# Optimization experiments

Hardware: AMD Instinct MI355X
Metric: run time of the kernel (lower is better)

## Reference

```python
import jax, jax.numpy as jnp
import numpy as np

DIM = 3
SIGMA_MIN = 0.05
NORM_EPS = 1e-10
DEG2RAD = np.pi / 180.0


def setup_inputs() -> dict:
    key = jax.random.key(0)
    kF, = jax.random.split(key, 1)
    B = 4_000_000
    F = jax.random.normal(kF, (B, 3, 3), dtype=jnp.float32)
    return {
        "F": F,
        "youngs_modulus_log": jnp.asarray(np.log(2_000_000.0), dtype=jnp.float32),
        "poissons_ratio": jnp.asarray(0.4, dtype=jnp.float32),
        "friction_angle": jnp.asarray(25.0, dtype=jnp.float32),
        "cohesion": jnp.asarray(0.0, dtype=jnp.float32),
    }


def reference(F, youngs_modulus_log, poissons_ratio, friction_angle, cohesion):
    E = jnp.exp(youngs_modulus_log)
    sin_phi = jnp.sin(friction_angle * DEG2RAD)
    alpha = jnp.sqrt(2.0 / 3.0) * 2.0 * sin_phi / (3.0 - sin_phi)
    mu = E / (2.0 * (1.0 + poissons_ratio))
    la = E * poissons_ratio / ((1.0 + poissons_ratio) * (1.0 - 2.0 * poissons_ratio))

    # Batched 3x3 SVD: U (B,3,3), sigma (B,3), Vh (B,3,3)
    U, sigma, Vh = jnp.linalg.svd(F, full_matrices=False)

    sigma = jnp.maximum(sigma, SIGMA_MIN)
    eps = jnp.log(sigma)                                   # log strain (B,3)
    trace = eps.sum(axis=1, keepdims=True)                 # (B,1)
    eps_hat = eps - trace / DIM                            # deviatoric part
    eps_hat_norm = jnp.maximum(
        jnp.linalg.norm(eps_hat, axis=1, keepdims=True), NORM_EPS)
    shifted_trace = trace - cohesion * DIM
    cond_yield = shifted_trace < 0.0                       # (B,1)
    delta_gamma = eps_hat_norm + (DIM * la + 2.0 * mu) / (2.0 * mu) * shifted_trace * alpha
    compress_eps = eps - jnp.maximum(delta_gamma, 0.0) / eps_hat_norm * eps_hat
    expand_eps = jnp.ones_like(eps) * cohesion
    eps_corrected = jnp.where(cond_yield, compress_eps, expand_eps)

    # F_corrected = U @ diag(exp(eps_corrected)) @ Vh
    F_corrected = jnp.einsum('bij,bj,bjk->bik', U, jnp.exp(eps_corrected), Vh)
    return F_corrected
```

## Files before the change

### kernel.cpp

```cpp
#include <hip/hip_runtime.h>
#include <math.h>

#define BLOCK 256
#define F4PB (BLOCK * 9 / 4)

__device__ __forceinline__ float frcp(float x)  { return __builtin_amdgcn_rcpf(x); }
__device__ __forceinline__ float frsq(float x)  { return __builtin_amdgcn_rsqf(x); }
__device__ __forceinline__ float fsqrt_r(float x){ return __builtin_amdgcn_sqrtf(x); }

__device__ __forceinline__ void rot(
    float& x0, float& x1, float& x2, float& np,
    float& y0, float& y1, float& y2, float& nq)
{
    float apq = fmaf(x0, y0, fmaf(x1, y1, x2 * y2));
    float del = np - nq;
    float rho = apq + apq;
    float r   = fsqrt_r(fmaf(del, del, rho * rho));
    float ch  = fabsf(del) + r + 1e-15f;
    bool  sw  = del < 0.0f;
    float sh  = sw ? -rho : rho;
    float inv = frsq(fmaf(ch, ch, sh * sh));
    float c   = ch * inv;
    float s   = sh * inv;
    float cf  = sw ? -s : c;
    float sf  = sw ?  c : s;
    float t;
    t = x0; x0 = fmaf(cf, t, sf * y0); y0 = fmaf(cf, y0, -sf * t);
    t = x1; x1 = fmaf(cf, t, sf * y1); y1 = fmaf(cf, y1, -sf * t);
    t = x2; x2 = fmaf(cf, t, sf * y2); y2 = fmaf(cf, y2, -sf * t);
    float sum = np + nq;
    np = 0.5f * (sum + r);
    nq = fmaxf(0.5f * (sum - r), 0.0f);
}

__global__ __launch_bounds__(BLOCK) void dp_kernel(
    const float* __restrict__ F,
    const float* __restrict__ p_yml,
    const float* __restrict__ p_nu,
    const float* __restrict__ p_fa,
    const float* __restrict__ p_coh,
    float* __restrict__ out,
    int n_elem)
{
    __shared__ float lds[BLOCK * 9];
    const int t_id    = threadIdx.x;
    const int nfloats = n_elem * 9;
    const int base_f  = (int)blockIdx.x * (BLOCK * 9);

    #pragma unroll
    for (int j = 0; j < 3; ++j) {
        int idx = t_id + j * BLOCK;
        if (idx < F4PB) {
            int g4 = (base_f >> 2) + idx;
            int gf = g4 << 2;
            if (gf + 4 <= nfloats) {
                ((float4*)lds)[idx] = ((const float4*)F)[g4];
            } else {
                #pragma unroll
                for (int k = 0; k < 4; ++k)
                    if (gf + k < nfloats) lds[idx * 4 + k] = F[gf + k];
            }
        }
    }
    __syncthreads();

    const int  e     = (int)blockIdx.x * BLOCK + t_id;
    const bool valid = e < n_elem;

    float a00, a01, a02, a10, a11, a12, a20, a21, a22;
    {
        const float* p = lds + t_id * 9;
        a00 = p[0]; a01 = p[1]; a02 = p[2];
        a10 = p[3]; a11 = p[4]; a12 = p[5];
        a20 = p[6]; a21 = p[7]; a22 = p[8];
    }

    const float yml = p_yml[0];
    const float nu  = p_nu[0];
    const float fa  = p_fa[0];
    const float coh = p_coh[0];
    const float E     = __expf(yml);
    const float sphi  = __sinf(fa * 0.017453292519943295f);
    const float alpha = 1.632993161855452f * sphi * frcp(3.0f - sphi);
    const float mu    = E * 0.5f * frcp(1.0f + nu);
    const float la    = E * nu * frcp((1.0f + nu) * (1.0f - 2.0f * nu));
    const float ratio = (3.0f * la + 2.0f * mu) * frcp(2.0f * mu) * alpha;

    float c00=a00, c10=a10, c20=a20;
    float c01=a01, c11=a11, c21=a21;
    float c02=a02, c12=a12, c22=a22;
    float n0 = fmaf(c00,c00, fmaf(c10,c10, c20*c20));
    float n1 = fmaf(c01,c01, fmaf(c11,c11, c21*c21));
    float n2 = fmaf(c02,c02, fmaf(c12,c12, c22*c22));

    #pragma unroll
    for (int sweep = 0; sweep < 4; ++sweep) {
        rot(c00,c10,c20,n0, c01,c11,c21,n1);
        rot(c00,c10,c20,n0, c02,c12,c22,n2);
        rot(c01,c11,c21,n1, c02,c12,c22,n2);
    }

    float i0 = frsq(fmaxf(n0, 1e-30f));
    float i1 = frsq(fmaxf(n1, 1e-30f));
    float u00 = c00*i0, u10 = c10*i0, u20 = c20*i0;
    float u01 = c01*i1, u11 = c11*i1, u21 = c21*i1;
    float u02 = fmaf(u10,u21, -u20*u11);
    float u12 = fmaf(u20,u01, -u00*u21);
    float u22 = fmaf(u00,u11, -u10*u01);

    float q0 = fmaf(a00,u00, fmaf(a10,u10, a20*u20));
    float q1 = fmaf(a01,u00, fmaf(a11,u10, a21*u20));
    float q2 = fmaf(a02,u00, fmaf(a12,u10, a22*u20));
    float m0 = fmaf(q0,q0, fmaf(q1,q1, q2*q2));
    float j0 = frsq(fmaxf(m0, 1e-30f));
    float v00 = q0*j0, v10 = q1*j0, v20 = q2*j0;

    q0 = fmaf(a00,u01, fmaf(a10,u11, a20*u21));
    q1 = fmaf(a01,u01, fmaf(a11,u11, a21*u21));
    q2 = fmaf(a02,u01, fmaf(a12,u11, a22*u21));
    float m1 = fmaf(q0,q0, fmaf(q1,q1, q2*q2));
    float j1 = frsq(fmaxf(m1, 1e-30f));
    float v01 = q0*j1, v11 = q1*j1, v21 = q2*j1;

    float v02 = fmaf(v10,v21, -v20*v11);
    float v12 = fmaf(v20,v01, -v00*v21);
    float v22 = fmaf(v00,v11, -v10*v01);

    float w0 = fmaf(a00,v02, fmaf(a01,v12, a02*v22));
    float w1 = fmaf(a10,v02, fmaf(a11,v12, a12*v22));
    float w2 = fmaf(a20,v02, fmaf(a21,v12, a22*v22));
    float s2 = fmaf(u02,w0, fmaf(u12,w1, u22*w2));

    float e0 = 0.5f * __logf(fmaxf(n0, 0.0025f));
    float e1 = 0.5f * __logf(fmaxf(n1, 0.0025f));
    float e2 = __logf(fmaxf(fabsf(s2), 0.05f));
    float tr  = e0 + e1 + e2;
    float tr3 = tr * (1.0f / 3.0f);
    float h0 = e0 - tr3, h1 = e1 - tr3, h2 = e2 - tr3;
    float hn = fsqrt_r(fmaf(h0,h0, fmaf(h1,h1, h2*h2)));
    hn = fmaxf(hn, 1e-10f);
    float st = tr - coh * 3.0f;
    float dg = hn + ratio * st;
    float sc = fmaxf(dg, 0.0f) * frcp(hn);
    bool yield = st < 0.0f;
    float ec0 = yield ? fmaf(-sc, h0, e0) : coh;
    float ec1 = yield ? fmaf(-sc, h1, e1) : coh;
    float ec2 = yield ? fmaf(-sc, h2, e2) : coh;
    float f0 = __expf(ec0);
    float f1 = __expf(ec1);
    float f2 = copysignf(__expf(ec2), s2);

    float w00 = u00*f0, w01 = u01*f1, w02 = u02*f2;
    float w10 = u10*f0, w11 = u11*f1, w12 = u12*f2;
    float w20 = u20*f0, w21 = u21*f1, w22 = u22*f2;
    float r00 = fmaf(w00,v00, fmaf(w01,v01, w02*v02));
    float r01 = fmaf(w00,v10, fmaf(w01,v11, w02*v12));
    float r02 = fmaf(w00,v20, fmaf(w01,v21, w02*v22));
    float r10 = fmaf(w10,v00, fmaf(w11,v01, w12*v02));
    float r11 = fmaf(w10,v10, fmaf(w11,v11, w12*v12));
    float r12 = fmaf(w10,v20, fmaf(w11,v21, w12*v22));
    float r20 = fmaf(w20,v00, fmaf(w21,v01, w22*v02));
    float r21 = fmaf(w20,v10, fmaf(w21,v11, w22*v12));
    float r22 = fmaf(w20,v20, fmaf(w21,v21, w22*v22));

    __syncthreads();
    if (valid) {
        float* p = lds + t_id * 9;
        p[0]=r00; p[1]=r01; p[2]=r02;
        p[3]=r10; p[4]=r11; p[5]=r12;
        p[6]=r20; p[7]=r21; p[8]=r22;
    }
    __syncthreads();

    #pragma unroll
    for (int j = 0; j < 3; ++j) {
        int idx = t_id + j * BLOCK;
        if (idx < F4PB) {
            int g4 = (base_f >> 2) + idx;
            int gf = g4 << 2;
            if (gf + 4 <= nfloats) {
                ((float4*)out)[g4] = ((float4*)lds)[idx];
            } else {
                #pragma unroll
                for (int k = 0; k < 4; ++k)
                    if (gf + k < nfloats) out[gf + k] = lds[idx * 4 + k];
            }
        }
    }
}

extern "C" void kernel_launch(void* const* d_in, const int* in_sizes, int n_in,
                              void* d_out, int out_size, void* d_ws, size_t ws_size,
                              hipStream_t stream) {
    const float* F = (const float*)d_in[0];
    const int n_elem = in_sizes[0] / 9;
    const int grid = (n_elem + BLOCK - 1) / BLOCK;
    dp_kernel<<<grid, BLOCK, 0, stream>>>(
        F,
        (const float*)d_in[1], (const float*)d_in[2],
        (const float*)d_in[3], (const float*)d_in[4],
        (float*)d_out, n_elem);
}
```

Baseline: 255.9 us.

## Replace Jacobi SVD with closed-form eigen solve, two elements per thread

Swaps the 4-sweep one-sided Jacobi SVD for an analytic eigendecomposition of F^T F (trigonometric cubic roots with a polynomial acos, plus cross-product eigenvectors), then recovers U from A·V. Each thread now handles two elements through a paired-float struct that the compiler may map to packed FP32 math. The LDS-staged coalesced float4 load/store is replaced by direct strided 9-float global accesses per element. The closed form can lose accuracy for nearly repeated or tiny singular values, and the uncoalesced memory access may hurt bandwidth on this memory-bound-sized problem.

```diff
diff --git a/kernel.cpp b/kernel.cpp
--- a/kernel.cpp
+++ b/kernel.cpp
@@ -2,38 +2,200 @@
 #include <math.h>
 
 #define BLOCK 256
-#define F4PB (BLOCK * 9 / 4)
-
-__device__ __forceinline__ float frcp(float x)  { return __builtin_amdgcn_rcpf(x); }
-__device__ __forceinline__ float frsq(float x)  { return __builtin_amdgcn_rsqf(x); }
+#define EPT   2
+#define EPB   (BLOCK * EPT)
+
+__device__ __forceinline__ float frcp(float x)   { return __builtin_amdgcn_rcpf(x); }
+__device__ __forceinline__ float frsq(float x)   { return __builtin_amdgcn_rsqf(x); }
 __device__ __forceinline__ float fsqrt_r(float x){ return __builtin_amdgcn_sqrtf(x); }
 
-__device__ __forceinline__ void rot(
-    float& x0, float& x1, float& x2, float& np,
-    float& y0, float& y1, float& y2, float& nq)
+struct v2f { float x, y; };
+struct m2  { bool  x, y; };
+
+__device__ __forceinline__ v2f mk2(float v)          { return {v, v}; }
+__device__ __forceinline__ v2f operator+(v2f a, v2f b){ return {a.x+b.x, a.y+b.y}; }
+__device__ __forceinline__ v2f operator-(v2f a, v2f b){ return {a.x-b.x, a.y-b.y}; }
+__device__ __forceinline__ v2f operator*(v2f a, v2f b){ return {a.x*b.x, a.y*b.y}; }
+__device__ __forceinline__ v2f operator-(v2f a)       { return {-a.x, -a.y}; }
+__device__ __forceinline__ v2f fma2(v2f a, v2f b, v2f c){ return {fmaf(a.x,b.x,c.x), fmaf(a.y,b.y,c.y)}; }
+__device__ __forceinline__ v2f max2(v2f a, v2f b)    { return {fmaxf(a.x,b.x), fmaxf(a.y,b.y)}; }
+__device__ __forceinline__ v2f min2(v2f a, v2f b)    { return {fminf(a.x,b.x), fminf(a.y,b.y)}; }
+__device__ __forceinline__ v2f abs2(v2f a)           { return {fabsf(a.x), fabsf(a.y)}; }
+__device__ __forceinline__ v2f rcp2(v2f a)           { return {frcp(a.x), frcp(a.y)}; }
+__device__ __forceinline__ v2f rsq2(v2f a)           { return {frsq(a.x), frsq(a.y)}; }
+__device__ __forceinline__ v2f sqrt2v(v2f a)         { return {fsqrt_r(a.x), fsqrt_r(a.y)}; }
+__device__ __forceinline__ v2f log2v(v2f a)          { return {__logf(a.x), __logf(a.y)}; }
+__device__ __forceinline__ v2f exp2v(v2f a)          { return {__expf(a.x), __expf(a.y)}; }
+__device__ __forceinline__ v2f cos2v(v2f a)          { return {__cosf(a.x), __cosf(a.y)}; }
+__device__ __forceinline__ v2f csign2(v2f a, v2f s)  { return {copysignf(a.x,s.x), copysignf(a.y,s.y)}; }
+__device__ __forceinline__ m2  lt2(v2f a, v2f b)     { return {a.x<b.x, a.y<b.y}; }
+__device__ __forceinline__ m2  gt2(v2f a, v2f b)     { return {a.x>b.x, a.y>b.y}; }
+__device__ __forceinline__ m2  le2(v2f a, v2f b)     { return {a.x<=b.x, a.y<=b.y}; }
+__device__ __forceinline__ m2  and2(m2 a, m2 b)      { return {a.x&&b.x, a.y&&b.y}; }
+__device__ __forceinline__ m2  or2(m2 a, m2 b)       { return {a.x||b.x, a.y||b.y}; }
+__device__ __forceinline__ m2  not2(m2 a)            { return {!a.x, !a.y}; }
+__device__ __forceinline__ v2f sel2(m2 m, v2f a, v2f b){ return {m.x?a.x:b.x, m.y?a.y:b.y}; }
+
+__device__ __forceinline__ v2f acos2(v2f v) {
+    v2f ax = abs2(v);
+    v2f p = fma2(ax, mk2(-0.0187293f), mk2(0.0742610f));
+    p = fma2(ax, p, mk2(-0.2121144f));
+    p = fma2(ax, p, mk2(1.5707288f));
+    v2f r = sqrt2v(max2(mk2(1.0f)-ax, mk2(0.0f))) * p;
+    return sel2(lt2(v, mk2(0.0f)), mk2(3.14159265358979f)-r, r);
+}
+
+__device__ __forceinline__ void best_cross2(
+    v2f r0x, v2f r0y, v2f r0z,
+    v2f r1x, v2f r1y, v2f r1z,
+    v2f r2x, v2f r2y, v2f r2z,
+    v2f& bx, v2f& by, v2f& bz, v2f& bn)
 {
-    float apq = fmaf(x0, y0, fmaf(x1, y1, x2 * y2));
-    float del = np - nq;
-    float rho = apq + apq;
-    float r   = fsqrt_r(fmaf(del, del, rho * rho));
-    float ch  = fabsf(del) + r + 1e-15f;
-    bool  sw  = del < 0.0f;
-    float sh  = sw ? -rho : rho;
-    float inv = frsq(fmaf(ch, ch, sh * sh));
-    float c   = ch * inv;
-    float s   = sh * inv;
-    float cf  = sw ? -s : c;
-    float sf  = sw ?  c : s;
-    float t;
-    t = x0; x0 = fmaf(cf, t, sf * y0); y0 = fmaf(cf, y0, -sf * t);
-    t = x1; x1 = fmaf(cf, t, sf * y1); y1 = fmaf(cf, y1, -sf * t);
-    t = x2; x2 = fmaf(cf, t, sf * y2); y2 = fmaf(cf, y2, -sf * t);
-    float sum = np + nq;
-    np = 0.5f * (sum + r);
-    nq = fmaxf(0.5f * (sum - r), 0.0f);
-}
-
-__global__ __launch_bounds__(BLOCK) void dp_kernel(
+    v2f c0x = fma2(r0y,r1z, -(r0z*r1y));
+    v2f c0y = fma2(r0z,r1x, -(r0x*r1z));
+    v2f c0z = fma2(r0x,r1y, -(r0y*r1x));
+    v2f c1x = fma2(r0y,r2z, -(r0z*r2y));
+    v2f c1y = fma2(r0z,r2x, -(r0x*r2z));
+    v2f c1z = fma2(r0x,r2y, -(r0y*r2x));
+    v2f c2x = fma2(r1y,r2z, -(r1z*r2y));
+    v2f c2y = fma2(r1z,r2x, -(r1x*r2z));
+    v2f c2z = fma2(r1x,r2y, -(r1y*r2x));
+    v2f n0 = fma2(c0x,c0x, fma2(c0y,c0y, c0z*c0z));
+    v2f n1 = fma2(c1x,c1x, fma2(c1y,c1y, c1z*c1z));
+    v2f n2 = fma2(c2x,c2x, fma2(c2y,c2y, c2z*c2z));
+    m2 b1 = gt2(n1, n0);
+    v2f sx = sel2(b1,c1x,c0x), sy = sel2(b1,c1y,c0y), sz = sel2(b1,c1z,c0z);
+    v2f sn = sel2(b1,n1,n0);
+    m2 b2m = gt2(n2, sn);
+    bx = sel2(b2m,c2x,sx); by = sel2(b2m,c2y,sy); bz = sel2(b2m,c2z,sz);
+    bn = sel2(b2m,n2,sn);
+}
+
+__device__ __forceinline__ void dp_solve2(
+    v2f a00, v2f a01, v2f a02,
+    v2f a10, v2f a11, v2f a12,
+    v2f a20, v2f a21, v2f a22,
+    float coh, float ratio,
+    v2f& r00, v2f& r01, v2f& r02,
+    v2f& r10, v2f& r11, v2f& r12,
+    v2f& r20, v2f& r21, v2f& r22)
+{
+    v2f s00 = fma2(a00,a00, fma2(a10,a10, a20*a20));
+    v2f s11 = fma2(a01,a01, fma2(a11,a11, a21*a21));
+    v2f s22 = fma2(a02,a02, fma2(a12,a12, a22*a22));
+    v2f s01 = fma2(a00,a01, fma2(a10,a11, a20*a21));
+    v2f s02 = fma2(a00,a02, fma2(a10,a12, a20*a22));
+    v2f s12 = fma2(a01,a02, fma2(a11,a12, a21*a22));
+
+    v2f q   = (s00 + s11 + s22) * mk2(1.0f/3.0f);
+    v2f b00 = s00 - q, b11 = s11 - q, b22 = s22 - q;
+    v2f offsq = fma2(s01,s01, fma2(s02,s02, s12*s12));
+    v2f p2  = fma2(b00,b00, fma2(b11,b11, fma2(b22,b22, mk2(2.0f)*offsq)));
+    v2f pp  = sqrt2v(p2 * mk2(1.0f/6.0f));
+    v2f pinv = rcp2(max2(pp, mk2(1e-10f)));
+    v2f det = b00*fma2(b11,b22, -(s12*s12))
+            - s01*fma2(s01,b22, -(s12*s02))
+            + s02*fma2(s01,s12, -(b11*s02));
+    v2f rdet = mk2(0.5f)*det*pinv*pinv*pinv;
+    rdet = min2(max2(rdet, mk2(-1.0f)), mk2(1.0f));
+    v2f phi  = acos2(rdet) * mk2(1.0f/3.0f);
+    v2f lam0 = fma2(mk2(2.0f)*pp, cos2v(phi), q);
+    v2f lam2 = fma2(mk2(2.0f)*pp, cos2v(phi + mk2(2.0943951023931953f)), q);
+
+    v2f bx, by, bz, bn;
+    best_cross2(s00-lam0, s01, s02,
+                s01, s11-lam0, s12,
+                s02, s12, s22-lam0, bx, by, bz, bn);
+    m2 ok0 = gt2(bn, mk2(1e-24f));
+    v2f ir0 = rsq2(max2(bn, mk2(1e-30f)));
+    v2f v00 = sel2(ok0, bx*ir0, mk2(1.0f));
+    v2f v10 = sel2(ok0, by*ir0, mk2(0.0f));
+    v2f v20 = sel2(ok0, bz*ir0, mk2(0.0f));
+
+    best_cross2(s00-lam2, s01, s02,
+                s01, s11-lam2, s12,
+                s02, s12, s22-lam2, bx, by, bz, bn);
+    v2f axv = abs2(v00), ayv = abs2(v10), azv = abs2(v20);
+    m2 xm = and2(le2(axv,ayv), le2(axv,azv));
+    m2 ym = and2(not2(xm), le2(ayv,azv));
+    m2 xym = or2(xm, ym);
+    v2f ex = sel2(xm, mk2(1.0f), mk2(0.0f));
+    v2f ey = sel2(ym, mk2(1.0f), mk2(0.0f));
+    v2f ez = sel2(xym, mk2(0.0f), mk2(1.0f));
+    v2f fx = fma2(v10,ez, -(v20*ey));
+    v2f fy = fma2(v20,ex, -(v00*ez));
+    v2f fz = fma2(v00,ey, -(v10*ex));
+    m2 ok2m = gt2(bn, mk2(1e-24f));
+    v2f wx = sel2(ok2m, bx, fx), wy = sel2(ok2m, by, fy), wz = sel2(ok2m, bz, fz);
+    v2f dp = fma2(wx,v00, fma2(wy,v10, wz*v20));
+    wx = fma2(-dp, v00, wx); wy = fma2(-dp, v10, wy); wz = fma2(-dp, v20, wz);
+    v2f wn = fma2(wx,wx, fma2(wy,wy, wz*wz));
+    m2 okw = gt2(wn, mk2(1e-24f));
+    wx = sel2(okw, wx, fx); wy = sel2(okw, wy, fy); wz = sel2(okw, wz, fz);
+    wn = sel2(okw, wn, fma2(fx,fx, fma2(fy,fy, fz*fz)));
+    v2f irw = rsq2(max2(wn, mk2(1e-30f)));
+    v2f v02 = wx*irw, v12 = wy*irw, v22 = wz*irw;
+    v2f v01 = fma2(v12,v20, -(v22*v10));
+    v2f v11 = fma2(v22,v00, -(v02*v20));
+    v2f v21 = fma2(v02,v10, -(v12*v00));
+
+    v2f q0 = fma2(a00,v00, fma2(a01,v10, a02*v20));
+    v2f q1 = fma2(a10,v00, fma2(a11,v10, a12*v20));
+    v2f q2 = fma2(a20,v00, fma2(a21,v10, a22*v20));
+    v2f m0 = fma2(q0,q0, fma2(q1,q1, q2*q2));
+    v2f i0 = rsq2(max2(m0, mk2(1e-30f)));
+    v2f u00 = q0*i0, u10 = q1*i0, u20 = q2*i0;
+
+    q0 = fma2(a00,v01, fma2(a01,v11, a02*v21));
+    q1 = fma2(a10,v01, fma2(a11,v11, a12*v21));
+    q2 = fma2(a20,v01, fma2(a21,v11, a22*v21));
+    v2f m1 = fma2(q0,q0, fma2(q1,q1, q2*q2));
+    v2f i1 = rsq2(max2(m1, mk2(1e-30f)));
+    v2f u01 = q0*i1, u11 = q1*i1, u21 = q2*i1;
+
+    v2f u02 = fma2(u10,u21, -(u20*u11));
+    v2f u12 = fma2(u20,u01, -(u00*u21));
+    v2f u22 = fma2(u00,u11, -(u10*u01));
+
+    v2f w0 = fma2(a00,v02, fma2(a01,v12, a02*v22));
+    v2f w1 = fma2(a10,v02, fma2(a11,v12, a12*v22));
+    v2f w2 = fma2(a20,v02, fma2(a21,v12, a22*v22));
+    v2f s2 = fma2(u02,w0, fma2(u12,w1, u22*w2));
+
+    v2f e0 = mk2(0.5f)*log2v(max2(m0, mk2(0.0025f)));
+    v2f e1 = mk2(0.5f)*log2v(max2(m1, mk2(0.0025f)));
+    v2f e2 = log2v(max2(abs2(s2), mk2(0.05f)));
+    v2f tr  = e0 + e1 + e2;
+    v2f tr3 = tr * mk2(1.0f/3.0f);
+    v2f h0 = e0 - tr3, h1 = e1 - tr3, h2 = e2 - tr3;
+    v2f hn = sqrt2v(fma2(h0,h0, fma2(h1,h1, h2*h2)));
+    hn = max2(hn, mk2(1e-10f));
+    v2f st = tr - mk2(coh*3.0f);
+    v2f dg = hn + mk2(ratio)*st;
+    v2f sc = max2(dg, mk2(0.0f)) * rcp2(hn);
+    m2 yield = lt2(st, mk2(0.0f));
+    v2f ec0 = sel2(yield, fma2(-sc, h0, e0), mk2(coh));
+    v2f ec1 = sel2(yield, fma2(-sc, h1, e1), mk2(coh));
+    v2f ec2 = sel2(yield, fma2(-sc, h2, e2), mk2(coh));
+    v2f g0 = exp2v(ec0);
+    v2f g1 = exp2v(ec1);
+    v2f g2 = csign2(exp2v(ec2), s2);
+
+    v2f w00 = u00*g0, w01 = u01*g1, w02 = u02*g2;
+    v2f w10 = u10*g0, w11 = u11*g1, w12 = u12*g2;
+    v2f w20 = u20*g0, w21 = u21*g1, w22 = u22*g2;
+    r00 = fma2(w00,v00, fma2(w01,v01, w02*v02));
+    r01 = fma2(w00,v10, fma2(w01,v11, w02*v12));
+    r02 = fma2(w00,v20, fma2(w01,v21, w02*v22));
+    r10 = fma2(w10,v00, fma2(w11,v01, w12*v02));
+    r11 = fma2(w10,v10, fma2(w11,v11, w12*v12));
+    r12 = fma2(w10,v20, fma2(w11,v21, w12*v22));
+    r20 = fma2(w20,v00, fma2(w21,v01, w22*v02));
+    r21 = fma2(w20,v10, fma2(w21,v11, w22*v12));
+    r22 = fma2(w20,v20, fma2(w21,v21, w22*v22));
+}
+
+__global__ __launch_bounds__(BLOCK, 4) void dp_kernel(
     const float* __restrict__ F,
     const float* __restrict__ p_yml,
     const float* __restrict__ p_nu,
@@ -42,38 +204,18 @@
     float* __restrict__ out,
     int n_elem)
 {
-    __shared__ float lds[BLOCK * 9];
-    const int t_id    = threadIdx.x;
-    const int nfloats = n_elem * 9;
-    const int base_f  = (int)blockIdx.x * (BLOCK * 9);
-
-    #pragma unroll
-    for (int j = 0; j < 3; ++j) {
-        int idx = t_id + j * BLOCK;
-        if (idx < F4PB) {
-            int g4 = (base_f >> 2) + idx;
-            int gf = g4 << 2;
-            if (gf + 4 <= nfloats) {
-                ((float4*)lds)[idx] = ((const float4*)F)[g4];
-            } else {
-                #pragma unroll
-                for (int k = 0; k < 4; ++k)
-                    if (gf + k < nfloats) lds[idx * 4 + k] = F[gf + k];
-            }
-        }
-    }
-    __syncthreads();
-
-    const int  e     = (int)blockIdx.x * BLOCK + t_id;
-    const bool valid = e < n_elem;
-
-    float a00, a01, a02, a10, a11, a12, a20, a21, a22;
-    {
-        const float* p = lds + t_id * 9;
-        a00 = p[0]; a01 = p[1]; a02 = p[2];
-        a10 = p[3]; a11 = p[4]; a12 = p[5];
-        a20 = p[6]; a21 = p[7]; a22 = p[8];
-    }
+    const int t    = threadIdx.x;
+    const int base = (int)blockIdx.x * EPB;
+    const int idxA = base + t;
+    const int idxB = base + BLOCK + t;
+    const bool vA = idxA < n_elem;
+    const bool vB = idxB < n_elem;
+    const float* pA = F + (vA ? idxA : 0) * 9;
+    const float* pB = F + (vB ? idxB : 0) * 9;
+
+    v2f a00 = {pA[0], pB[0]}, a01 = {pA[1], pB[1]}, a02 = {pA[2], pB[2]};
+    v2f a10 = {pA[3], pB[3]}, a11 = {pA[4], pB[4]}, a12 = {pA[5], pB[5]};
+    v2f a20 = {pA[6], pB[6]}, a21 = {pA[7], pB[7]}, a22 = {pA[8], pB[8]};
 
     const float yml = p_yml[0];
     const float nu  = p_nu[0];
@@ -86,106 +228,21 @@
     const float la    = E * nu * frcp((1.0f + nu) * (1.0f - 2.0f * nu));
     const float ratio = (3.0f * la + 2.0f * mu) * frcp(2.0f * mu) * alpha;
 
-    float c00=a00, c10=a10, c20=a20;
-    float c01=a01, c11=a11, c21=a21;
-    float c02=a02, c12=a12, c22=a22;
-    float n0 = fmaf(c00,c00, fmaf(c10,c10, c20*c20));
-    float n1 = fmaf(c01,c01, fmaf(c11,c11, c21*c21));
-    float n2 = fmaf(c02,c02, fmaf(c12,c12, c22*c22));
-
-    #pragma unroll
-    for (int sweep = 0; sweep < 4; ++sweep) {
-        rot(c00,c10,c20,n0, c01,c11,c21,n1);
-        rot(c00,c10,c20,n0, c02,c12,c22,n2);
-        rot(c01,c11,c21,n1, c02,c12,c22,n2);
+    v2f r00,r01,r02,r10,r11,r12,r20,r21,r22;
+    dp_solve2(a00,a01,a02,a10,a11,a12,a20,a21,a22, coh, ratio,
+              r00,r01,r02,r10,r11,r12,r20,r21,r22);
+
+    if (vA) {
+        float* o = out + idxA * 9;
+        o[0]=r00.x; o[1]=r01.x; o[2]=r02.x;
+        o[3]=r10.x; o[4]=r11.x; o[5]=r12.x;
+        o[6]=r20.x; o[7]=r21.x; o[8]=r22.x;
     }
-
-    float i0 = frsq(fmaxf(n0, 1e-30f));
-    float i1 = frsq(fmaxf(n1, 1e-30f));
-    float u00 = c00*i0, u10 = c10*i0, u20 = c20*i0;
-    float u01 = c01*i1, u11 = c11*i1, u21 = c21*i1;
-    float u02 = fmaf(u10,u21, -u20*u11);
-    float u12 = fmaf(u20,u01, -u00*u21);
-    float u22 = fmaf(u00,u11, -u10*u01);
-
-    float q0 = fmaf(a00,u00, fmaf(a10,u10, a20*u20));
-    float q1 = fmaf(a01,u00, fmaf(a11,u10, a21*u20));
-    float q2 = fmaf(a02,u00, fmaf(a12,u10, a22*u20));
-    float m0 = fmaf(q0,q0, fmaf(q1,q1, q2*q2));
-    float j0 = frsq(fmaxf(m0, 1e-30f));
-    float v00 = q0*j0, v10 = q1*j0, v20 = q2*j0;
-
-    q0 = fmaf(a00,u01, fmaf(a10,u11, a20*u21));
-    q1 = fmaf(a01,u01, fmaf(a11,u11, a21*u21));
-    q2 = fmaf(a02,u01, fmaf(a12,u11, a22*u21));
-    float m1 = fmaf(q0,q0, fmaf(q1,q1, q2*q2));
-    float j1 = frsq(fmaxf(m1, 1e-30f));
-    float v01 = q0*j1, v11 = q1*j1, v21 = q2*j1;
-
-    float v02 = fmaf(v10,v21, -v20*v11);
-    float v12 = fmaf(v20,v01, -v00*v21);
-    float v22 = fmaf(v00,v11, -v10*v01);
-
-    float w0 = fmaf(a00,v02, fmaf(a01,v12, a02*v22));
-    float w1 = fmaf(a10,v02, fmaf(a11,v12, a12*v22));
-    float w2 = fmaf(a20,v02, fmaf(a21,v12, a22*v22));
-    float s2 = fmaf(u02,w0, fmaf(u12,w1, u22*w2));
-
-    float e0 = 0.5f * __logf(fmaxf(n0, 0.0025f));
-    float e1 = 0.5f * __logf(fmaxf(n1, 0.0025f));
-    float e2 = __logf(fmaxf(fabsf(s2), 0.05f));
-    float tr  = e0 + e1 + e2;
-    float tr3 = tr * (1.0f / 3.0f);
-    float h0 = e0 - tr3, h1 = e1 - tr3, h2 = e2 - tr3;
-    float hn = fsqrt_r(fmaf(h0,h0, fmaf(h1,h1, h2*h2)));
-    hn = fmaxf(hn, 1e-10f);
-    float st = tr - coh * 3.0f;
-    float dg = hn + ratio * st;
-    float sc = fmaxf(dg, 0.0f) * frcp(hn);
-    bool yield = st < 0.0f;
-    float ec0 = yield ? fmaf(-sc, h0, e0) : coh;
-    float ec1 = yield ? fmaf(-sc, h1, e1) : coh;
-    float ec2 = yield ? fmaf(-sc, h2, e2) : coh;
-    float f0 = __expf(ec0);
-    float f1 = __expf(ec1);
-    float f2 = copysignf(__expf(ec2), s2);
-
-    float w00 = u00*f0, w01 = u01*f1, w02 = u02*f2;
-    float w10 = u10*f0, w11 = u11*f1, w12 = u12*f2;
-    float w20 = u20*f0, w21 = u21*f1, w22 = u22*f2;
-    float r00 = fmaf(w00,v00, fmaf(w01,v01, w02*v02));
-    float r01 = fmaf(w00,v10, fmaf(w01,v11, w02*v12));
-    float r02 = fmaf(w00,v20, fmaf(w01,v21, w02*v22));
-    float r10 = fmaf(w10,v00, fmaf(w11,v01, w12*v02));
-    float r11 = fmaf(w10,v10, fmaf(w11,v11, w12*v12));
-    float r12 = fmaf(w10,v20, fmaf(w11,v21, w12*v22));
-    float r20 = fmaf(w20,v00, fmaf(w21,v01, w22*v02));
-    float r21 = fmaf(w20,v10, fmaf(w21,v11, w22*v12));
-    float r22 = fmaf(w20,v20, fmaf(w21,v21, w22*v22));
-
-    __syncthreads();
-    if (valid) {
-        float* p = lds + t_id * 9;
-        p[0]=r00; p[1]=r01; p[2]=r02;
-        p[3]=r10; p[4]=r11; p[5]=r12;
-        p[6]=r20; p[7]=r21; p[8]=r22;
-    }
-    __syncthreads();
-
-    #pragma unroll
-    for (int j = 0; j < 3; ++j) {
-        int idx = t_id + j * BLOCK;
-        if (idx < F4PB) {
-            int g4 = (base_f >> 2) + idx;
-            int gf = g4 << 2;
-            if (gf + 4 <= nfloats) {
-                ((float4*)out)[g4] = ((float4*)lds)[idx];
-            } else {
-                #pragma unroll
-                for (int k = 0; k < 4; ++k)
-                    if (gf + k < nfloats) out[gf + k] = lds[idx * 4 + k];
-            }
-        }
+    if (vB) {
+        float* o = out + idxB * 9;
+        o[0]=r00.y; o[1]=r01.y; o[2]=r02.y;
+        o[3]=r10.y; o[4]=r11.y; o[5]=r12.y;
+        o[6]=r20.y; o[7]=r21.y; o[8]=r22.y;
     }
 }
 
@@ -194,7 +251,7 @@
                               hipStream_t stream) {
     const float* F = (const float*)d_in[0];
     const int n_elem = in_sizes[0] / 9;
-    const int grid = (n_elem + BLOCK - 1) / BLOCK;
+    const int grid = (n_elem + EPB - 1) / EPB;
     dp_kernel<<<grid, BLOCK, 0, stream>>>(
         F,
         (const float*)d_in[1], (const float*)d_in[2],
```

Measured after the change: 258.0 us. No clear change (+0.8%).
